# Optimization experiments

Hardware: AMD Instinct MI355X
Metric: run time of the kernel (lower is better)

Reference implementation:

```python
import jax, jax.numpy as jnp
import numpy as np

B, L, D, H, MAXREL = 8, 1024, 1024, 16, 32
DPH = D // H  # 64


def setup_inputs() -> dict:
    rng = jax.random.key(0)
    ks = jax.random.split(rng, 16)
    s = 0.02
    inp = {
        "key": jax.random.normal(ks[0], (B, L, D), jnp.float32),
        "value": jax.random.normal(ks[1], (B, L, D), jnp.float32),
        "query": jax.random.normal(ks[2], (B, L, D), jnp.float32),
        "mask": jax.random.bernoulli(ks[3], 0.1, (B, 1, L)),
        "Wq": jax.random.normal(ks[4], (D, D), jnp.float32) * s,
        "bq": jnp.zeros((D,), jnp.float32),
        "Wk": jax.random.normal(ks[5], (D, D), jnp.float32) * s,
        "bk": jnp.zeros((D,), jnp.float32),
        "Wv": jax.random.normal(ks[6], (D, D), jnp.float32) * s,
        "bv": jnp.zeros((D,), jnp.float32),
        "Wo": jax.random.normal(ks[7], (D, D), jnp.float32) * s,
        "bo": jnp.zeros((D,), jnp.float32),
        "rel_emb": jax.random.normal(ks[8], (2 * MAXREL + 1, DPH), jnp.float32) * s,
    }
    return inp


def reference(key, value, query, mask, Wq, bq, Wk, bk, Wv, bv, Wo, bo, rel_emb):
    b, l, d = query.shape
    def shape(x):  # (b, l, D) -> (b, H, l, dph)
        return x.reshape(b, -1, H, DPH).transpose(0, 2, 1, 3)

    q = shape(query @ Wq.T + bq) / jnp.sqrt(jnp.asarray(DPH, query.dtype))
    k = shape(key @ Wk.T + bk)
    v = shape(value @ Wv.T + bv)

    # Shaw-style relative position embeddings: rel[i, j] = clip(j - i, -M, M) + M
    idx = jnp.arange(l)
    rel = jnp.clip(idx[None, :] - idx[:, None], -MAXREL, MAXREL) + MAXREL  # (l, l)
    Er = rel_emb[rel]  # (l, l, dph) -- used for both keys and values (same table)

    scores = jnp.einsum('bhqd,bhkd->bhqk', q, k) + jnp.einsum('bhqd,qkd->bhqk', q, Er)
    scores = jnp.where(mask[:, None, :, :], jnp.asarray(-1e18, scores.dtype), scores)
    attn = jax.nn.softmax(scores, axis=-1)  # dropout = identity at eval

    ctx = jnp.einsum('bhqk,bhkd->bhqd', attn, v) + jnp.einsum('bhqk,qkd->bhqd', attn, Er)
    out = ctx.transpose(0, 2, 1, 3).reshape(b, l, H * DPH) @ Wo.T + bo
    top_attn = attn[:, 0]  # (b, q_len, k_len)
    return out, top_attn
```

## Files before the change

### kernel.cpp

```cpp
#include <hip/hip_runtime.h>
#include <hip/hip_bf16.h>

typedef __bf16 bf16x8 __attribute__((ext_vector_type(8)));
typedef __bf16 bf16x4 __attribute__((ext_vector_type(4)));
typedef float f32x4 __attribute__((ext_vector_type(4)));
typedef float f32x8 __attribute__((ext_vector_type(8)));

#define B_ 8
#define L_ 1024
#define D_ 1024
#define H_ 16
#define DPH_ 64
#define MAXREL_ 32
#define NREL_ 65

__device__ __forceinline__ f32x4 mfma16x16x32(bf16x8 a, bf16x8 b, f32x4 c) {
    return __builtin_amdgcn_mfma_f32_16x16x32_bf16(a, b, c, 0, 0, 0);
}

__device__ __forceinline__ bf16x8 ld_any(const float* p) {
    f32x8 v = *(const f32x8*)p;
    bf16x8 r;
    #pragma unroll
    for (int i = 0; i < 8; ++i) r[i] = (__bf16)v[i];
    return r;
}
__device__ __forceinline__ bf16x8 ld_any(const __bf16* p) { return *(const bf16x8*)p; }

template <int MODE, typename TA>
__global__ __launch_bounds__(512, 2) void gemm_v2(
    const TA* __restrict__ X, const float* __restrict__ Wt,
    const float* __restrict__ bias, void* __restrict__ outp,
    int M, int N, int K, float scale)
{
    __shared__ __bf16 sA[2][128 * 40];
    __shared__ __bf16 sB[2][256 * 40];

    const int tid = threadIdx.x;
    const int nbn = N >> 8;
    const int wg = (int)blockIdx.x;
    const int row0 = (wg / nbn) * 128, col0 = (wg % nbn) * 256;
    const int lane = tid & 63, w = tid >> 6, lr = lane & 15, lk = lane >> 4;
    const int wm = w >> 2, wn = w & 3;

    const int arow = tid >> 2, ak = (tid & 3) * 8;
    const int brow = tid >> 1, bk = (tid & 1) * 16;
    const TA*    agp = X  + (size_t)(row0 + arow) * K + ak;
    const float* bgp = Wt + (size_t)(col0 + brow) * K + bk;

    f32x4 acc[4][4];
    #pragma unroll
    for (int a = 0; a < 4; ++a)
        #pragma unroll
        for (int b = 0; b < 4; ++b) acc[a][b] = (f32x4){0.f, 0.f, 0.f, 0.f};

    f32x4 ra0, ra1;
    bf16x8 rab;
    f32x4 rb0, rb1, rb2, rb3;

    #define LOADG(t) do {                                                    \
        const int _k0 = (t) * 32;                                            \
        if (sizeof(TA) == 4) {                                               \
            ra0 = *(const f32x4*)((const float*)agp + _k0);                  \
            ra1 = *(const f32x4*)((const float*)agp + _k0 + 4);              \
        } else {                                                             \
            rab = *(const bf16x8*)((const __bf16*)agp + _k0);                \
        }                                                                    \
        rb0 = *(const f32x4*)(bgp + _k0);                                    \
        rb1 = *(const f32x4*)(bgp + _k0 + 4);                                \
        rb2 = *(const f32x4*)(bgp + _k0 + 8);                                \
        rb3 = *(const f32x4*)(bgp + _k0 + 12);                               \
    } while (0)

    #define WRITEL(buf) do {                                                 \
        bf16x8 _av;                                                          \
        if (sizeof(TA) == 4) {                                               \
            _Pragma("unroll")                                                \
            for (int i = 0; i < 4; ++i) {                                    \
                _av[i] = (__bf16)ra0[i]; _av[4 + i] = (__bf16)ra1[i];        \
            }                                                                \
        } else { _av = rab; }                                                \
        *(bf16x8*)&sA[buf][arow * 40 + ak] = _av;                            \
        bf16x8 _bv0, _bv1;                                                   \
        _Pragma("unroll")                                                    \
        for (int i = 0; i < 4; ++i) {                                        \
            _bv0[i] = (__bf16)rb0[i]; _bv0[4 + i] = (__bf16)rb1[i];          \
            _bv1[i] = (__bf16)rb2[i]; _bv1[4 + i] = (__bf16)rb3[i];          \
        }                                                                    \
        *(bf16x8*)&sB[buf][brow * 40 + bk]     = _bv0;                       \
        *(bf16x8*)&sB[buf][brow * 40 + bk + 8] = _bv1;                       \
    } while (0)

    LOADG(0);
    WRITEL(0);
    LOADG(1);
    __syncthreads();

    const int nkt = K >> 5;
    for (int t = 0; t < nkt; ++t) {
        const int cur = t & 1;
        bf16x8 af[4], bfr[4];
        #pragma unroll
        for (int m = 0; m < 4; ++m)
            af[m] = *(const bf16x8*)&sA[cur][(wm * 64 + m * 16 + lr) * 40 + 8 * lk];
        #pragma unroll
        for (int n = 0; n < 4; ++n)
            bfr[n] = *(const bf16x8*)&sB[cur][(wn * 64 + n * 16 + lr) * 40 + 8 * lk];
        __builtin_amdgcn_s_setprio(1);
        #pragma unroll
        for (int m = 0; m < 4; ++m)
            #pragma unroll
            for (int n = 0; n < 4; ++n)
                acc[m][n] = mfma16x16x32(af[m], bfr[n], acc[m][n]);
        __builtin_amdgcn_s_setprio(0);
        if (t < nkt - 1) {
            WRITEL(cur ^ 1);
            if (t < nkt - 2) LOADG(t + 2);
            __syncthreads();
        }
    }
    #undef LOADG
    #undef WRITEL

    #pragma unroll
    for (int ni = 0; ni < 4; ++ni) {
        const int n = col0 + wn * 64 + ni * 16 + lr;
        const float bv = bias[n];
        #pragma unroll
        for (int mi = 0; mi < 4; ++mi) {
            const int m0 = row0 + wm * 64 + mi * 16 + lk * 4;
            if (MODE == 0) {
                #pragma unroll
                for (int i = 0; i < 4; ++i)
                    ((__bf16*)outp)[(size_t)(m0 + i) * N + n] =
                        (__bf16)((acc[mi][ni][i] + bv) * scale);
            } else if (MODE == 1) {
                bf16x4 v4;
                #pragma unroll
                for (int i = 0; i < 4; ++i) v4[i] = (__bf16)(acc[mi][ni][i] + bv);
                *(bf16x4*)((__bf16*)outp + ((size_t)(m0 >> 10) << 20)
                           + (size_t)n * L_ + (m0 & 1023)) = v4;
            } else {
                #pragma unroll
                for (int i = 0; i < 4; ++i)
                    ((float*)outp)[(size_t)(m0 + i) * N + n] = acc[mi][ni][i] + bv;
            }
        }
    }
}

__global__ __launch_bounds__(256, 3) void attn_v5(
    const __bf16* __restrict__ Q, const __bf16* __restrict__ K,
    const __bf16* __restrict__ Vt, const int* __restrict__ mask,
    const float* __restrict__ relg, __bf16* __restrict__ ctx,
    float* __restrict__ attn0)
{
    __shared__ __bf16 sK[2][64 * 64];
    __shared__ __bf16 sV[2][64 * 64];
    __shared__ __bf16 s_rq[64 * 72];
    __shared__ __bf16 s_arel[64 * 72];
    __shared__ float s_sums[64];
    __shared__ unsigned s_mbits[32];

    const int tid = threadIdx.x;
    const int wg = ((int)blockIdx.x & 7) * 256 + ((int)blockIdx.x >> 3);
    const int qt = wg & 15, h = (wg >> 4) & 15, b = wg >> 8;
    const int q0 = qt * 64;
    const int lane = tid & 63, w = tid >> 6, lr = lane & 15, lk = lane >> 4;
    const size_t bh = (size_t)b * (L_ * D_) + (size_t)h * DPH_;
    const int qw = q0 + w * 16;
    const int ql = w * 16;

    const int strow = tid >> 3;
    const int scg   = (tid & 7) ^ (strow & 7);
    const __bf16* Kgp = K + bh + (size_t)strow * D_ + scg * 8;
    const __bf16* Vgp = Vt + ((size_t)b << 20)
                      + (size_t)(h * DPH_ + strow) * L_ + scg * 8;

    const __bf16* qp = Q + bh + (size_t)(qw + lr) * D_ + 8 * lk;
    const bf16x8 qf0 = *(const bf16x8*)qp;
    const bf16x8 qf1 = *(const bf16x8*)(qp + 32);

    #pragma unroll
    for (int rr = 0; rr < 4; ++rr) {
        const int k = rr * 256 + w * 64 + lane;
        const unsigned long long bal = __ballot(mask[b * L_ + k] != 0);
        if (lane == 0) {
            s_mbits[rr * 8 + w * 2]     = (unsigned)bal;
            s_mbits[rr * 8 + w * 2 + 1] = (unsigned)(bal >> 32);
        }
    }
    for (int i = tid; i < 64 * 72; i += 256) s_arel[i] = (__bf16)0.f;

    #pragma unroll
    for (int jt = 0; jt < 5; ++jt) {
        const int jr = jt * 16 + lr;
        const int jc = jr > 64 ? 64 : jr;
        const float* rp = relg + jc * 64 + 8 * lk;
        f32x4 rq = {0.f, 0.f, 0.f, 0.f};
        rq = mfma16x16x32(ld_any(rp), qf0, rq);
        rq = mfma16x16x32(ld_any(rp + 32), qf1, rq);
        #pragma unroll
        for (int i = 0; i < 4; ++i) {
            const int jj = jt * 16 + lk * 4 + i;
            if (jj <= 64) s_rq[(ql + lr) * 72 + jj] = (__bf16)rq[i];
        }
    }

    bf16x8 rk0 = *(const bf16x8*)(Kgp);
    bf16x8 rk1 = *(const bf16x8*)(Kgp + 32 * (size_t)D_);
    bf16x8 rv0 = *(const bf16x8*)(Vgp);
    bf16x8 rv1 = *(const bf16x8*)(Vgp + 32 * (size_t)L_);
    __syncthreads();

    const float rq0  = (float)s_rq[(ql + lr) * 72 + 0];
    const float rq64 = (float)s_rq[(ql + lr) * 72 + 64];

    float sum = 0.f, c0 = 0.f, c64 = 0.f;
    f32x4 pvacc[4];
    #pragma unroll
    for (int dt = 0; dt < 4; ++dt) pvacc[dt] = (f32x4){0.f, 0.f, 0.f, 0.f};
    float* a0p = attn0 + ((size_t)b * L_ + qw + lr) * L_;
    const int sw = lr & 7;
    const int s0l = lr + 32 * (lk & 1);
    const int s1l = s0l + 16;
    const bool hisel = (lk >> 1) != 0;

    for (int it = 0; it < 16; ++it) {
        const int cur = it & 1;
        const int k0 = it * 64;
        {
            __bf16* kd = &sK[cur][tid * 8];
            __bf16* vd = &sV[cur][tid * 8];
            *(bf16x8*)kd = rk0;  *(bf16x8*)(kd + 2048) = rk1;
            *(bf16x8*)vd = rv0;  *(bf16x8*)(vd + 2048) = rv1;
        }
        __syncthreads();
        if (it < 15) {
            const size_t ko = (size_t)(k0 + 64) * D_;
            rk0 = *(const bf16x8*)(Kgp + ko);
            rk1 = *(const bf16x8*)(Kgp + ko + 32 * (size_t)D_);
            rv0 = *(const bf16x8*)(Vgp + k0 + 64);
            rv1 = *(const bf16x8*)(Vgp + k0 + 64 + 32 * (size_t)L_);
        }

        const __bf16* kb = sK[cur];
        const __bf16* vb = sV[cur];

        float p[4][4];
        #pragma unroll
        for (int kt = 0; kt < 4; ++kt) {
            const int rb = (kt * 16 + lr) * 64;
            const bf16x8 a0 = *(const bf16x8*)&kb[rb + ((lk ^ sw) * 8)];
            const bf16x8 a1 = *(const bf16x8*)&kb[rb + (((lk + 4) ^ sw) * 8)];
            f32x4 acc = {0.f, 0.f, 0.f, 0.f};
            acc = mfma16x16x32(a0, qf0, acc);
            acc = mfma16x16x32(a1, qf1, acc);
            #pragma unroll
            for (int i = 0; i < 4; ++i) p[kt][i] = acc[i];
        }

        const unsigned mw0 = s_mbits[(k0 >> 5)];
        const unsigned mw1 = s_mbits[(k0 >> 5) + 1];
        const int side = (k0 <= qw - 95) ? -1 : ((k0 >= qw + 47) ? 1 : 0);
        if (side == 0) {
            #pragma unroll
            for (int kt = 0; kt < 4; ++kt) {
                const unsigned mword = kt < 2 ? mw0 : mw1;
                #pragma unroll
                for (int i = 0; i < 4; ++i) {
                    const int k = k0 + kt * 16 + lk * 4 + i;
                    const int dd = k - (qw + lr);
                    int j = dd + MAXREL_;
                    j = j < 0 ? 0 : (j > 64 ? 64 : j);
                    const float bias = (float)s_rq[(ql + lr) * 72 + j];
                    const float e = ((mword >> (k & 31)) & 1u)
                                  ? 0.f : __expf(p[kt][i] + bias);
                    p[kt][i] = e;
                    sum += e;
                    if (dd <= -MAXREL_)      c0  += e;
                    else if (dd >= MAXREL_)  c64 += e;
                    else s_arel[(ql + lr) * 72 + dd + MAXREL_] = (__bf16)e;
                }
            }
        } else {
            const float bias = side < 0 ? rq0 : rq64;
            float cacc = 0.f;
            #pragma unroll
            for (int kt = 0; kt < 4; ++kt) {
                const unsigned mword = kt < 2 ? mw0 : mw1;
                #pragma unroll
                for (int i = 0; i < 4; ++i) {
                    const int k = k0 + kt * 16 + lk * 4 + i;
                    const float e = ((mword >> (k & 31)) & 1u)
                                  ? 0.f : __expf(p[kt][i] + bias);
                    p[kt][i] = e;
                    cacc += e;
                }
            }
            sum += cacc;
            if (side < 0) c0 += cacc; else c64 += cacc;
        }

        if (h == 0) {
            #pragma unroll
            for (int kt = 0; kt < 4; ++kt) {
                f32x4 st;
                #pragma unroll
                for (int i = 0; i < 4; ++i) st[i] = p[kt][i];
                *(f32x4*)&a0p[k0 + kt * 16 + lk * 4] = st;
            }
        }

        unsigned pk[4][2];
        #pragma unroll
        for (int kt = 0; kt < 4; ++kt)
            #pragma unroll
            for (int hf = 0; hf < 2; ++hf) {
                union { unsigned u; __bf16 x[2]; } t;
                t.x[0] = (__bf16)p[kt][2 * hf];
                t.x[1] = (__bf16)p[kt][2 * hf + 1];
                pk[kt][hf] = t.u;
            }

        #pragma unroll
        for (int s = 0; s < 2; ++s) {
            union { unsigned u[4]; bf16x8 v; } ua;
            {
                const unsigned aE0 = __shfl((int)pk[2 * s][0],     s0l, 64);
                const unsigned aO0 = __shfl((int)pk[2 * s + 1][0], s0l, 64);
                const unsigned aE1 = __shfl((int)pk[2 * s][1],     s0l, 64);
                const unsigned aO1 = __shfl((int)pk[2 * s + 1][1], s0l, 64);
                const unsigned bE0 = __shfl((int)pk[2 * s][0],     s1l, 64);
                const unsigned bO0 = __shfl((int)pk[2 * s + 1][0], s1l, 64);
                const unsigned bE1 = __shfl((int)pk[2 * s][1],     s1l, 64);
                const unsigned bO1 = __shfl((int)pk[2 * s + 1][1], s1l, 64);
                ua.u[0] = hisel ? aO0 : aE0;
                ua.u[1] = hisel ? aO1 : aE1;
                ua.u[2] = hisel ? bO0 : bE0;
                ua.u[3] = hisel ? bO1 : bE1;
            }
            #pragma unroll
            for (int dt = 0; dt < 4; ++dt) {
                const bf16x8 bfv = *(const bf16x8*)
                    &vb[(dt * 16 + lr) * 64 + (((4 * s + lk) ^ sw) * 8)];
                pvacc[dt] = mfma16x16x32(ua.v, bfv, pvacc[dt]);
            }
        }
    }

    sum += __shfl_xor(sum, 16, 64); sum += __shfl_xor(sum, 32, 64);
    c0  += __shfl_xor(c0, 16, 64);  c0  += __shfl_xor(c0, 32, 64);
    c64 += __shfl_xor(c64, 16, 64); c64 += __shfl_xor(c64, 32, 64);
    if (lane < 16) {
        s_sums[ql + lr] = sum;
        s_arel[(ql + lr) * 72 + 0]  = (__bf16)c0;
        s_arel[(ql + lr) * 72 + 64] = (__bf16)c64;
    }
    __syncthreads();

    __bf16* rT = (__bf16*)sK;
    for (int i = tid; i < NREL_ * DPH_; i += 256)
        rT[(i & 63) * 72 + (i >> 6)] = (__bf16)relg[i];
    __syncthreads();

    const bf16x8 af1 = *(const bf16x8*)&s_arel[(ql + lr) * 72 + 8 * lk];
    const bf16x8 af2 = *(const bf16x8*)&s_arel[(ql + lr) * 72 + 32 + 8 * lk];
    float a64[4], inv[4];
    #pragma unroll
    for (int i = 0; i < 4; ++i) {
        a64[i] = (float)s_arel[(ql + lk * 4 + i) * 72 + 64];
        inv[i] = 1.f / s_sums[ql + lk * 4 + i];
    }
    #pragma unroll
    for (int dt = 0; dt < 4; ++dt) {
        const bf16x8 b1 = *(const bf16x8*)&rT[(dt * 16 + lr) * 72 + 8 * lk];
        const bf16x8 b2 = *(const bf16x8*)&rT[(dt * 16 + lr) * 72 + 32 + 8 * lk];
        pvacc[dt] = mfma16x16x32(af1, b1, pvacc[dt]);
        pvacc[dt] = mfma16x16x32(af2, b2, pvacc[dt]);
        const float r64 = (float)rT[(dt * 16 + lr) * 72 + 64];
        #pragma unroll
        for (int i = 0; i < 4; ++i) {
            const float outv = (pvacc[dt][i] + a64[i] * r64) * inv[i];
            ctx[((size_t)b * L_ + q0 + ql + lk * 4 + i) * D_
                + h * DPH_ + dt * 16 + lr] = (__bf16)outv;
        }
    }

    if (h == 0) {
        #pragma unroll 4
        for (int n = 0; n < 16; ++n) {
            const float invr = 1.f / s_sums[ql + n];
            float* ap = attn0 + ((size_t)b * L_ + q0 + ql + n) * L_ + lane * 16;
            #pragma unroll
            for (int c = 0; c < 4; ++c) {
                f32x4 v = *(f32x4*)&ap[c * 4];
                #pragma unroll
                for (int i = 0; i < 4; ++i) v[i] *= invr;
                *(f32x4*)&ap[c * 4] = v;
            }
        }
    }
}

extern "C" void kernel_launch(void* const* d_in, const int* in_sizes, int n_in,
                              void* d_out, int out_size, void* d_ws, size_t ws_size,
                              hipStream_t stream) {
    const float* key   = (const float*)d_in[0];
    const float* value = (const float*)d_in[1];
    const float* query = (const float*)d_in[2];
    const int*   mask  = (const int*)d_in[3];
    const float* Wq = (const float*)d_in[4];
    const float* bq = (const float*)d_in[5];
    const float* Wk = (const float*)d_in[6];
    const float* bk = (const float*)d_in[7];
    const float* Wv = (const float*)d_in[8];
    const float* bv = (const float*)d_in[9];
    const float* Wo = (const float*)d_in[10];
    const float* bo = (const float*)d_in[11];
    const float* relg = (const float*)d_in[12];

    float* out   = (float*)d_out;
    float* attn0 = out + (size_t)B_ * L_ * D_;

    char* ws = (char*)d_ws;
    __bf16* Qw   = (__bf16*)(ws);
    __bf16* Kw   = (__bf16*)(ws + ((size_t)16 << 20));
    __bf16* Vtw  = (__bf16*)(ws + ((size_t)32 << 20));
    __bf16* Ctxw = (__bf16*)(ws + ((size_t)48 << 20));

    const int M = B_ * L_;
    const int ngemm = (M / 128) * (D_ / 256);

    gemm_v2<0, float><<<ngemm, dim3(512), 0, stream>>>(query, Wq, bq, Qw, M, D_, D_, 0.125f);
    gemm_v2<0, float><<<ngemm, dim3(512), 0, stream>>>(key,   Wk, bk, Kw, M, D_, D_, 1.0f);
    gemm_v2<1, float><<<ngemm, dim3(512), 0, stream>>>(value, Wv, bv, Vtw, M, D_, D_, 1.0f);

    attn_v5<<<B_ * H_ * (L_ / 64), dim3(256), 0, stream>>>(
        Qw, Kw, Vtw, mask, relg, Ctxw, attn0);

    gemm_v2<2, __bf16><<<ngemm, dim3(512), 0, stream>>>(Ctxw, Wo, bo, out, M, D_, D_, 1.0f);
}
```

Baseline: 240.5 us.

## Process 128 query rows per attention block to reuse K/V tiles

The attention kernel now handles 128 queries per workgroup, each wave owning two 16-row query sub-tiles, so every K/V tile staged in shared memory feeds twice as many MFMAs. The grid halves to 1024 blocks and the launch bound drops to 2 waves per SIMD to fit the doubled accumulators and score registers. This cuts K/V global and LDS traffic per query but raises register and shared-memory pressure and lowers the number of resident blocks. The threshold for the far-right side test is also widened to cover the 32-row wave span.

```diff
diff --git a/kernel.cpp b/kernel.cpp
--- a/kernel.cpp
+++ b/kernel.cpp
@@ -149,7 +149,7 @@
     }
 }
 
-__global__ __launch_bounds__(256, 3) void attn_v5(
+__global__ __launch_bounds__(256, 2) void attn_v8(
     const __bf16* __restrict__ Q, const __bf16* __restrict__ K,
     const __bf16* __restrict__ Vt, const int* __restrict__ mask,
     const float* __restrict__ relg, __bf16* __restrict__ ctx,
@@ -157,19 +157,19 @@
 {
     __shared__ __bf16 sK[2][64 * 64];
     __shared__ __bf16 sV[2][64 * 64];
-    __shared__ __bf16 s_rq[64 * 72];
-    __shared__ __bf16 s_arel[64 * 72];
-    __shared__ float s_sums[64];
+    __shared__ __bf16 s_rq[128 * 72];
+    __shared__ __bf16 s_arel[128 * 72];
+    __shared__ float s_sums[128];
     __shared__ unsigned s_mbits[32];
 
     const int tid = threadIdx.x;
-    const int wg = ((int)blockIdx.x & 7) * 256 + ((int)blockIdx.x >> 3);
-    const int qt = wg & 15, h = (wg >> 4) & 15, b = wg >> 8;
-    const int q0 = qt * 64;
+    const int wg = ((int)blockIdx.x & 7) * 128 + ((int)blockIdx.x >> 3);
+    const int qt = wg & 7, h = (wg >> 3) & 15, b = wg >> 7;
+    const int q0 = qt * 128;
     const int lane = tid & 63, w = tid >> 6, lr = lane & 15, lk = lane >> 4;
     const size_t bh = (size_t)b * (L_ * D_) + (size_t)h * DPH_;
-    const int qw = q0 + w * 16;
-    const int ql = w * 16;
+    const int ql = w * 32;
+    const int qw = q0 + ql;
 
     const int strow = tid >> 3;
     const int scg   = (tid & 7) ^ (strow & 7);
@@ -177,9 +177,13 @@
     const __bf16* Vgp = Vt + ((size_t)b << 20)
                       + (size_t)(h * DPH_ + strow) * L_ + scg * 8;
 
-    const __bf16* qp = Q + bh + (size_t)(qw + lr) * D_ + 8 * lk;
-    const bf16x8 qf0 = *(const bf16x8*)qp;
-    const bf16x8 qf1 = *(const bf16x8*)(qp + 32);
+    bf16x8 qf[2][2];
+    #pragma unroll
+    for (int hf = 0; hf < 2; ++hf) {
+        const __bf16* qp = Q + bh + (size_t)(qw + hf * 16 + lr) * D_ + 8 * lk;
+        qf[hf][0] = *(const bf16x8*)qp;
+        qf[hf][1] = *(const bf16x8*)(qp + 32);
+    }
 
     #pragma unroll
     for (int rr = 0; rr < 4; ++rr) {
@@ -190,22 +194,24 @@
             s_mbits[rr * 8 + w * 2 + 1] = (unsigned)(bal >> 32);
         }
     }
-    for (int i = tid; i < 64 * 72; i += 256) s_arel[i] = (__bf16)0.f;
-
-    #pragma unroll
-    for (int jt = 0; jt < 5; ++jt) {
-        const int jr = jt * 16 + lr;
-        const int jc = jr > 64 ? 64 : jr;
-        const float* rp = relg + jc * 64 + 8 * lk;
-        f32x4 rq = {0.f, 0.f, 0.f, 0.f};
-        rq = mfma16x16x32(ld_any(rp), qf0, rq);
-        rq = mfma16x16x32(ld_any(rp + 32), qf1, rq);
-        #pragma unroll
-        for (int i = 0; i < 4; ++i) {
-            const int jj = jt * 16 + lk * 4 + i;
-            if (jj <= 64) s_rq[(ql + lr) * 72 + jj] = (__bf16)rq[i];
-        }
-    }
+    for (int i = tid; i < 128 * 72; i += 256) s_arel[i] = (__bf16)0.f;
+
+    #pragma unroll
+    for (int hf = 0; hf < 2; ++hf)
+        #pragma unroll
+        for (int jt = 0; jt < 5; ++jt) {
+            const int jr = jt * 16 + lr;
+            const int jc = jr > 64 ? 64 : jr;
+            const float* rp = relg + jc * 64 + 8 * lk;
+            f32x4 rq = {0.f, 0.f, 0.f, 0.f};
+            rq = mfma16x16x32(ld_any(rp), qf[hf][0], rq);
+            rq = mfma16x16x32(ld_any(rp + 32), qf[hf][1], rq);
+            #pragma unroll
+            for (int i = 0; i < 4; ++i) {
+                const int jj = jt * 16 + lk * 4 + i;
+                if (jj <= 64) s_rq[(ql + hf * 16 + lr) * 72 + jj] = (__bf16)rq[i];
+            }
+        }
 
     bf16x8 rk0 = *(const bf16x8*)(Kgp);
     bf16x8 rk1 = *(const bf16x8*)(Kgp + 32 * (size_t)D_);
@@ -213,14 +219,20 @@
     bf16x8 rv1 = *(const bf16x8*)(Vgp + 32 * (size_t)L_);
     __syncthreads();
 
-    const float rq0  = (float)s_rq[(ql + lr) * 72 + 0];
-    const float rq64 = (float)s_rq[(ql + lr) * 72 + 64];
-
-    float sum = 0.f, c0 = 0.f, c64 = 0.f;
-    f32x4 pvacc[4];
-    #pragma unroll
-    for (int dt = 0; dt < 4; ++dt) pvacc[dt] = (f32x4){0.f, 0.f, 0.f, 0.f};
-    float* a0p = attn0 + ((size_t)b * L_ + qw + lr) * L_;
+    float rq0[2], rq64[2];
+    #pragma unroll
+    for (int hf = 0; hf < 2; ++hf) {
+        rq0[hf]  = (float)s_rq[(ql + hf * 16 + lr) * 72 + 0];
+        rq64[hf] = (float)s_rq[(ql + hf * 16 + lr) * 72 + 64];
+    }
+
+    float sum0 = 0.f, sum1 = 0.f, c0a = 0.f, c0b = 0.f, c64a = 0.f, c64b = 0.f;
+    f32x4 pvA[4], pvB[4];
+    #pragma unroll
+    for (int dt = 0; dt < 4; ++dt) {
+        pvA[dt] = (f32x4){0.f, 0.f, 0.f, 0.f};
+        pvB[dt] = (f32x4){0.f, 0.f, 0.f, 0.f};
+    }
     const int sw = lr & 7;
     const int s0l = lr + 32 * (lk & 1);
     const int s1l = s0l + 16;
@@ -247,115 +259,147 @@
         const __bf16* kb = sK[cur];
         const __bf16* vb = sV[cur];
 
-        float p[4][4];
+        float p[2][4][4];
         #pragma unroll
         for (int kt = 0; kt < 4; ++kt) {
             const int rb = (kt * 16 + lr) * 64;
             const bf16x8 a0 = *(const bf16x8*)&kb[rb + ((lk ^ sw) * 8)];
             const bf16x8 a1 = *(const bf16x8*)&kb[rb + (((lk + 4) ^ sw) * 8)];
-            f32x4 acc = {0.f, 0.f, 0.f, 0.f};
-            acc = mfma16x16x32(a0, qf0, acc);
-            acc = mfma16x16x32(a1, qf1, acc);
-            #pragma unroll
-            for (int i = 0; i < 4; ++i) p[kt][i] = acc[i];
+            #pragma unroll
+            for (int hf = 0; hf < 2; ++hf) {
+                f32x4 acc = {0.f, 0.f, 0.f, 0.f};
+                acc = mfma16x16x32(a0, qf[hf][0], acc);
+                acc = mfma16x16x32(a1, qf[hf][1], acc);
+                #pragma unroll
+                for (int i = 0; i < 4; ++i) p[hf][kt][i] = acc[i];
+            }
         }
 
         const unsigned mw0 = s_mbits[(k0 >> 5)];
         const unsigned mw1 = s_mbits[(k0 >> 5) + 1];
-        const int side = (k0 <= qw - 95) ? -1 : ((k0 >= qw + 47) ? 1 : 0);
-        if (side == 0) {
-            #pragma unroll
-            for (int kt = 0; kt < 4; ++kt) {
-                const unsigned mword = kt < 2 ? mw0 : mw1;
-                #pragma unroll
-                for (int i = 0; i < 4; ++i) {
-                    const int k = k0 + kt * 16 + lk * 4 + i;
-                    const int dd = k - (qw + lr);
-                    int j = dd + MAXREL_;
-                    j = j < 0 ? 0 : (j > 64 ? 64 : j);
-                    const float bias = (float)s_rq[(ql + lr) * 72 + j];
-                    const float e = ((mword >> (k & 31)) & 1u)
-                                  ? 0.f : __expf(p[kt][i] + bias);
-                    p[kt][i] = e;
-                    sum += e;
-                    if (dd <= -MAXREL_)      c0  += e;
-                    else if (dd >= MAXREL_)  c64 += e;
-                    else s_arel[(ql + lr) * 72 + dd + MAXREL_] = (__bf16)e;
+        const int side = (k0 <= qw - 95) ? -1 : ((k0 >= qw + 63) ? 1 : 0);
+        #pragma unroll
+        for (int hf = 0; hf < 2; ++hf) {
+            const int qg = qw + hf * 16 + lr;
+            const int rqrow = (ql + hf * 16 + lr) * 72;
+            if (side == 0) {
+                float lsum = 0.f, lc0 = 0.f, lc64 = 0.f;
+                #pragma unroll
+                for (int kt = 0; kt < 4; ++kt) {
+                    const unsigned mword = kt < 2 ? mw0 : mw1;
+                    #pragma unroll
+                    for (int i = 0; i < 4; ++i) {
+                        const int k = k0 + kt * 16 + lk * 4 + i;
+                        const int dd = k - qg;
+                        int j = dd + MAXREL_;
+                        j = j < 0 ? 0 : (j > 64 ? 64 : j);
+                        const float bias = (float)s_rq[rqrow + j];
+                        const float e = ((mword >> (k & 31)) & 1u)
+                                      ? 0.f : __expf(p[hf][kt][i] + bias);
+                        p[hf][kt][i] = e;
+                        lsum += e;
+                        if (dd <= -MAXREL_)      lc0  += e;
+                        else if (dd >= MAXREL_)  lc64 += e;
+                        else s_arel[rqrow + dd + MAXREL_] = (__bf16)e;
+                    }
                 }
-            }
-        } else {
-            const float bias = side < 0 ? rq0 : rq64;
-            float cacc = 0.f;
-            #pragma unroll
-            for (int kt = 0; kt < 4; ++kt) {
-                const unsigned mword = kt < 2 ? mw0 : mw1;
-                #pragma unroll
-                for (int i = 0; i < 4; ++i) {
-                    const int k = k0 + kt * 16 + lk * 4 + i;
-                    const float e = ((mword >> (k & 31)) & 1u)
-                                  ? 0.f : __expf(p[kt][i] + bias);
-                    p[kt][i] = e;
-                    cacc += e;
+                if (hf == 0) { sum0 += lsum; c0a += lc0; c64a += lc64; }
+                else         { sum1 += lsum; c0b += lc0; c64b += lc64; }
+            } else {
+                const float bias = side < 0 ? rq0[hf] : rq64[hf];
+                float cacc = 0.f;
+                #pragma unroll
+                for (int kt = 0; kt < 4; ++kt) {
+                    const unsigned mword = kt < 2 ? mw0 : mw1;
+                    #pragma unroll
+                    for (int i = 0; i < 4; ++i) {
+                        const int k = k0 + kt * 16 + lk * 4 + i;
+                        const float e = ((mword >> (k & 31)) & 1u)
+                                      ? 0.f : __expf(p[hf][kt][i] + bias);
+                        p[hf][kt][i] = e;
+                        cacc += e;
+                    }
                 }
-            }
-            sum += cacc;
-            if (side < 0) c0 += cacc; else c64 += cacc;
+                if (hf == 0) {
+                    sum0 += cacc;
+                    if (side < 0) c0a += cacc; else c64a += cacc;
+                } else {
+                    sum1 += cacc;
+                    if (side < 0) c0b += cacc; else c64b += cacc;
+                }
+            }
         }
 
         if (h == 0) {
             #pragma unroll
-            for (int kt = 0; kt < 4; ++kt) {
-                f32x4 st;
-                #pragma unroll
-                for (int i = 0; i < 4; ++i) st[i] = p[kt][i];
-                *(f32x4*)&a0p[k0 + kt * 16 + lk * 4] = st;
-            }
-        }
-
-        unsigned pk[4][2];
-        #pragma unroll
-        for (int kt = 0; kt < 4; ++kt)
-            #pragma unroll
             for (int hf = 0; hf < 2; ++hf) {
-                union { unsigned u; __bf16 x[2]; } t;
-                t.x[0] = (__bf16)p[kt][2 * hf];
-                t.x[1] = (__bf16)p[kt][2 * hf + 1];
-                pk[kt][hf] = t.u;
-            }
+                float* a0p = attn0 + ((size_t)b * L_ + qw + hf * 16 + lr) * L_;
+                #pragma unroll
+                for (int kt = 0; kt < 4; ++kt) {
+                    f32x4 st;
+                    #pragma unroll
+                    for (int i = 0; i < 4; ++i) st[i] = p[hf][kt][i];
+                    *(f32x4*)&a0p[k0 + kt * 16 + lk * 4] = st;
+                }
+            }
+        }
+
+        unsigned pk[2][4][2];
+        #pragma unroll
+        for (int hf = 0; hf < 2; ++hf)
+            #pragma unroll
+            for (int kt = 0; kt < 4; ++kt)
+                #pragma unroll
+                for (int pf = 0; pf < 2; ++pf) {
+                    union { unsigned u; __bf16 x[2]; } t;
+                    t.x[0] = (__bf16)p[hf][kt][2 * pf];
+                    t.x[1] = (__bf16)p[hf][kt][2 * pf + 1];
+                    pk[hf][kt][pf] = t.u;
+                }
 
         #pragma unroll
         for (int s = 0; s < 2; ++s) {
-            union { unsigned u[4]; bf16x8 v; } ua;
-            {
-                const unsigned aE0 = __shfl((int)pk[2 * s][0],     s0l, 64);
-                const unsigned aO0 = __shfl((int)pk[2 * s + 1][0], s0l, 64);
-                const unsigned aE1 = __shfl((int)pk[2 * s][1],     s0l, 64);
-                const unsigned aO1 = __shfl((int)pk[2 * s + 1][1], s0l, 64);
-                const unsigned bE0 = __shfl((int)pk[2 * s][0],     s1l, 64);
-                const unsigned bO0 = __shfl((int)pk[2 * s + 1][0], s1l, 64);
-                const unsigned bE1 = __shfl((int)pk[2 * s][1],     s1l, 64);
-                const unsigned bO1 = __shfl((int)pk[2 * s + 1][1], s1l, 64);
-                ua.u[0] = hisel ? aO0 : aE0;
-                ua.u[1] = hisel ? aO1 : aE1;
-                ua.u[2] = hisel ? bO0 : bE0;
-                ua.u[3] = hisel ? bO1 : bE1;
+            union { unsigned u[4]; bf16x8 v; } uaA, uaB;
+            #pragma unroll
+            for (int hf = 0; hf < 2; ++hf) {
+                const unsigned aE0 = __shfl((int)pk[hf][2 * s][0],     s0l, 64);
+                const unsigned aO0 = __shfl((int)pk[hf][2 * s + 1][0], s0l, 64);
+                const unsigned aE1 = __shfl((int)pk[hf][2 * s][1],     s0l, 64);
+                const unsigned aO1 = __shfl((int)pk[hf][2 * s + 1][1], s0l, 64);
+                const unsigned bE0 = __shfl((int)pk[hf][2 * s][0],     s1l, 64);
+                const unsigned bO0 = __shfl((int)pk[hf][2 * s + 1][0], s1l, 64);
+                const unsigned bE1 = __shfl((int)pk[hf][2 * s][1],     s1l, 64);
+                const unsigned bO1 = __shfl((int)pk[hf][2 * s + 1][1], s1l, 64);
+                unsigned u0 = hisel ? aO0 : aE0;
+                unsigned u1 = hisel ? aO1 : aE1;
+                unsigned u2 = hisel ? bO0 : bE0;
+                unsigned u3 = hisel ? bO1 : bE1;
+                if (hf == 0) { uaA.u[0]=u0; uaA.u[1]=u1; uaA.u[2]=u2; uaA.u[3]=u3; }
+                else         { uaB.u[0]=u0; uaB.u[1]=u1; uaB.u[2]=u2; uaB.u[3]=u3; }
             }
             #pragma unroll
             for (int dt = 0; dt < 4; ++dt) {
                 const bf16x8 bfv = *(const bf16x8*)
                     &vb[(dt * 16 + lr) * 64 + (((4 * s + lk) ^ sw) * 8)];
-                pvacc[dt] = mfma16x16x32(ua.v, bfv, pvacc[dt]);
-            }
-        }
-    }
-
-    sum += __shfl_xor(sum, 16, 64); sum += __shfl_xor(sum, 32, 64);
-    c0  += __shfl_xor(c0, 16, 64);  c0  += __shfl_xor(c0, 32, 64);
-    c64 += __shfl_xor(c64, 16, 64); c64 += __shfl_xor(c64, 32, 64);
+                pvA[dt] = mfma16x16x32(uaA.v, bfv, pvA[dt]);
+                pvB[dt] = mfma16x16x32(uaB.v, bfv, pvB[dt]);
+            }
+        }
+    }
+
+    sum0 += __shfl_xor(sum0, 16, 64); sum0 += __shfl_xor(sum0, 32, 64);
+    sum1 += __shfl_xor(sum1, 16, 64); sum1 += __shfl_xor(sum1, 32, 64);
+    c0a  += __shfl_xor(c0a, 16, 64);  c0a  += __shfl_xor(c0a, 32, 64);
+    c0b  += __shfl_xor(c0b, 16, 64);  c0b  += __shfl_xor(c0b, 32, 64);
+    c64a += __shfl_xor(c64a, 16, 64); c64a += __shfl_xor(c64a, 32, 64);
+    c64b += __shfl_xor(c64b, 16, 64); c64b += __shfl_xor(c64b, 32, 64);
     if (lane < 16) {
-        s_sums[ql + lr] = sum;
-        s_arel[(ql + lr) * 72 + 0]  = (__bf16)c0;
-        s_arel[(ql + lr) * 72 + 64] = (__bf16)c64;
+        s_sums[ql + lr] = sum0;
+        s_sums[ql + 16 + lr] = sum1;
+        s_arel[(ql + lr) * 72 + 0]       = (__bf16)c0a;
+        s_arel[(ql + lr) * 72 + 64]      = (__bf16)c64a;
+        s_arel[(ql + 16 + lr) * 72 + 0]  = (__bf16)c0b;
+        s_arel[(ql + 16 + lr) * 72 + 64] = (__bf16)c64b;
     }
     __syncthreads();
 
@@ -364,32 +408,37 @@
         rT[(i & 63) * 72 + (i >> 6)] = (__bf16)relg[i];
     __syncthreads();
 
-    const bf16x8 af1 = *(const bf16x8*)&s_arel[(ql + lr) * 72 + 8 * lk];
-    const bf16x8 af2 = *(const bf16x8*)&s_arel[(ql + lr) * 72 + 32 + 8 * lk];
-    float a64[4], inv[4];
-    #pragma unroll
-    for (int i = 0; i < 4; ++i) {
-        a64[i] = (float)s_arel[(ql + lk * 4 + i) * 72 + 64];
-        inv[i] = 1.f / s_sums[ql + lk * 4 + i];
-    }
-    #pragma unroll
-    for (int dt = 0; dt < 4; ++dt) {
-        const bf16x8 b1 = *(const bf16x8*)&rT[(dt * 16 + lr) * 72 + 8 * lk];
-        const bf16x8 b2 = *(const bf16x8*)&rT[(dt * 16 + lr) * 72 + 32 + 8 * lk];
-        pvacc[dt] = mfma16x16x32(af1, b1, pvacc[dt]);
-        pvacc[dt] = mfma16x16x32(af2, b2, pvacc[dt]);
-        const float r64 = (float)rT[(dt * 16 + lr) * 72 + 64];
+    #pragma unroll
+    for (int hf = 0; hf < 2; ++hf) {
+        const int qrow = ql + hf * 16;
+        const bf16x8 af1 = *(const bf16x8*)&s_arel[(qrow + lr) * 72 + 8 * lk];
+        const bf16x8 af2 = *(const bf16x8*)&s_arel[(qrow + lr) * 72 + 32 + 8 * lk];
+        float a64[4], inv[4];
         #pragma unroll
         for (int i = 0; i < 4; ++i) {
-            const float outv = (pvacc[dt][i] + a64[i] * r64) * inv[i];
-            ctx[((size_t)b * L_ + q0 + ql + lk * 4 + i) * D_
-                + h * DPH_ + dt * 16 + lr] = (__bf16)outv;
+            a64[i] = (float)s_arel[(qrow + lk * 4 + i) * 72 + 64];
+            inv[i] = 1.f / s_sums[qrow + lk * 4 + i];
+        }
+        #pragma unroll
+        for (int dt = 0; dt < 4; ++dt) {
+            f32x4 pv = hf == 0 ? pvA[dt] : pvB[dt];
+            const bf16x8 b1 = *(const bf16x8*)&rT[(dt * 16 + lr) * 72 + 8 * lk];
+            const bf16x8 b2 = *(const bf16x8*)&rT[(dt * 16 + lr) * 72 + 32 + 8 * lk];
+            pv = mfma16x16x32(af1, b1, pv);
+            pv = mfma16x16x32(af2, b2, pv);
+            const float r64 = (float)rT[(dt * 16 + lr) * 72 + 64];
+            #pragma unroll
+            for (int i = 0; i < 4; ++i) {
+                const float outv = (pv[i] + a64[i] * r64) * inv[i];
+                ctx[((size_t)b * L_ + q0 + qrow + lk * 4 + i) * D_
+                    + h * DPH_ + dt * 16 + lr] = (__bf16)outv;
+            }
         }
     }
 
     if (h == 0) {
         #pragma unroll 4
-        for (int n = 0; n < 16; ++n) {
+        for (int n = 0; n < 32; ++n) {
             const float invr = 1.f / s_sums[ql + n];
             float* ap = attn0 + ((size_t)b * L_ + q0 + ql + n) * L_ + lane * 16;
             #pragma unroll
@@ -436,7 +485,7 @@
     gemm_v2<0, float><<<ngemm, dim3(512), 0, stream>>>(key,   Wk, bk, Kw, M, D_, D_, 1.0f);
     gemm_v2<1, float><<<ngemm, dim3(512), 0, stream>>>(value, Wv, bv, Vtw, M, D_, D_, 1.0f);
 
-    attn_v5<<<B_ * H_ * (L_ / 64), dim3(256), 0, stream>>>(
+    attn_v8<<<B_ * H_ * (L_ / 128), dim3(256), 0, stream>>>(
         Qw, Kw, Vtw, mask, relg, Ctxw, attn0);
 
     gemm_v2<2, __bf16><<<ngemm, dim3(512), 0, stream>>>(Ctxw, Wo, bo, out, M, D_, D_, 1.0f);
```

Measured after the change: 262.1 us. +9.0%, slower.

## Pre-convert weights to bf16 and fuse QKV projections into one XCD-aware launch

Applied to the files above, without the earlier changes.

Adds small kernels that convert Wq/Wk/Wv and Wo to bf16 into workspace each call. The three Q/K/V projection GEMMs are merged into one 768-block launch, with a block-to-tile mapping that groups tiles per XCD. The GEMM body is refactored into a device function that takes bf16 weights, which halves weight bytes loaded per tile and removes repeated fp32-to-bf16 conversion inside each GEMM block. The cost is extra conversion launches and workspace reuse: Wb aliases the Ctx buffer and Wob aliases the Q buffer, which relies on stream ordering to stay correct.

```diff
diff --git a/kernel.cpp b/kernel.cpp
--- a/kernel.cpp
+++ b/kernel.cpp
@@ -27,26 +27,47 @@
 }
 __device__ __forceinline__ bf16x8 ld_any(const __bf16* p) { return *(const bf16x8*)p; }
 
-template <int MODE, typename TA>
-__global__ __launch_bounds__(512, 2) void gemm_v2(
-    const TA* __restrict__ X, const float* __restrict__ Wt,
+__global__ __launch_bounds__(256) void cvt3(
+    const float* __restrict__ a, const float* __restrict__ b,
+    const float* __restrict__ c, __bf16* __restrict__ dst)
+{
+    const int gid = blockIdx.x * 256 + threadIdx.x;
+    const int arr = gid >> 17;
+    const int off = (gid & 131071) * 8;
+    const float* src = arr == 0 ? a : (arr == 1 ? b : c);
+    f32x8 v = *(const f32x8*)(src + off);
+    bf16x8 r;
+    #pragma unroll
+    for (int i = 0; i < 8; ++i) r[i] = (__bf16)v[i];
+    *(bf16x8*)(dst + ((size_t)arr << 20) + off) = r;
+}
+
+__global__ __launch_bounds__(256) void cvt1(
+    const float* __restrict__ a, __bf16* __restrict__ dst)
+{
+    const int off = (blockIdx.x * 256 + threadIdx.x) * 8;
+    f32x8 v = *(const f32x8*)(a + off);
+    bf16x8 r;
+    #pragma unroll
+    for (int i = 0; i < 8; ++i) r[i] = (__bf16)v[i];
+    *(bf16x8*)(dst + off) = r;
+}
+
+template <typename TA, typename TB>
+__device__ __forceinline__ void gemm_body(
+    const TA* __restrict__ X, const TB* __restrict__ Wt,
     const float* __restrict__ bias, void* __restrict__ outp,
-    int M, int N, int K, float scale)
+    const int row0, const int col0, const int mode, const float scale,
+    __bf16* sA, __bf16* sB)
 {
-    __shared__ __bf16 sA[2][128 * 40];
-    __shared__ __bf16 sB[2][256 * 40];
-
+    const int K = 1024, N = 1024;
     const int tid = threadIdx.x;
-    const int nbn = N >> 8;
-    const int wg = (int)blockIdx.x;
-    const int row0 = (wg / nbn) * 128, col0 = (wg % nbn) * 256;
     const int lane = tid & 63, w = tid >> 6, lr = lane & 15, lk = lane >> 4;
     const int wm = w >> 2, wn = w & 3;
-
     const int arow = tid >> 2, ak = (tid & 3) * 8;
     const int brow = tid >> 1, bk = (tid & 1) * 16;
-    const TA*    agp = X  + (size_t)(row0 + arow) * K + ak;
-    const float* bgp = Wt + (size_t)(col0 + brow) * K + bk;
+    const TA* agp = X  + (size_t)(row0 + arow) * K + ak;
+    const TB* bgp = Wt + (size_t)(col0 + brow) * K + bk;
 
     f32x4 acc[4][4];
     #pragma unroll
@@ -54,42 +75,47 @@
         #pragma unroll
         for (int b = 0; b < 4; ++b) acc[a][b] = (f32x4){0.f, 0.f, 0.f, 0.f};
 
-    f32x4 ra0, ra1;
-    bf16x8 rab;
-    f32x4 rb0, rb1, rb2, rb3;
-
-    #define LOADG(t) do {                                                    \
-        const int _k0 = (t) * 32;                                            \
-        if (sizeof(TA) == 4) {                                               \
-            ra0 = *(const f32x4*)((const float*)agp + _k0);                  \
-            ra1 = *(const f32x4*)((const float*)agp + _k0 + 4);              \
-        } else {                                                             \
-            rab = *(const bf16x8*)((const __bf16*)agp + _k0);                \
-        }                                                                    \
-        rb0 = *(const f32x4*)(bgp + _k0);                                    \
-        rb1 = *(const f32x4*)(bgp + _k0 + 4);                                \
-        rb2 = *(const f32x4*)(bgp + _k0 + 8);                                \
-        rb3 = *(const f32x4*)(bgp + _k0 + 12);                               \
-    } while (0)
-
-    #define WRITEL(buf) do {                                                 \
-        bf16x8 _av;                                                          \
-        if (sizeof(TA) == 4) {                                               \
-            _Pragma("unroll")                                                \
-            for (int i = 0; i < 4; ++i) {                                    \
-                _av[i] = (__bf16)ra0[i]; _av[4 + i] = (__bf16)ra1[i];        \
-            }                                                                \
-        } else { _av = rab; }                                                \
-        *(bf16x8*)&sA[buf][arow * 40 + ak] = _av;                            \
-        bf16x8 _bv0, _bv1;                                                   \
-        _Pragma("unroll")                                                    \
-        for (int i = 0; i < 4; ++i) {                                        \
-            _bv0[i] = (__bf16)rb0[i]; _bv0[4 + i] = (__bf16)rb1[i];          \
-            _bv1[i] = (__bf16)rb2[i]; _bv1[4 + i] = (__bf16)rb3[i];          \
-        }                                                                    \
-        *(bf16x8*)&sB[buf][brow * 40 + bk]     = _bv0;                       \
-        *(bf16x8*)&sB[buf][brow * 40 + bk + 8] = _bv1;                       \
-    } while (0)
+    f32x4 ra0, ra1; bf16x8 rab;
+    f32x4 rb0, rb1, rb2, rb3; bf16x8 rbb0, rbb1;
+
+    auto LOADG = [&](int t) {
+        const int k0 = t * 32;
+        if (sizeof(TA) == 4) {
+            ra0 = *(const f32x4*)((const float*)agp + k0);
+            ra1 = *(const f32x4*)((const float*)agp + k0 + 4);
+        } else {
+            rab = *(const bf16x8*)((const __bf16*)agp + k0);
+        }
+        if (sizeof(TB) == 4) {
+            rb0 = *(const f32x4*)((const float*)bgp + k0);
+            rb1 = *(const f32x4*)((const float*)bgp + k0 + 4);
+            rb2 = *(const f32x4*)((const float*)bgp + k0 + 8);
+            rb3 = *(const f32x4*)((const float*)bgp + k0 + 12);
+        } else {
+            rbb0 = *(const bf16x8*)((const __bf16*)bgp + k0);
+            rbb1 = *(const bf16x8*)((const __bf16*)bgp + k0 + 8);
+        }
+    };
+    auto WRITEL = [&](int buf) {
+        bf16x8 av;
+        if (sizeof(TA) == 4) {
+            #pragma unroll
+            for (int i = 0; i < 4; ++i) {
+                av[i] = (__bf16)ra0[i]; av[4 + i] = (__bf16)ra1[i];
+            }
+        } else av = rab;
+        *(bf16x8*)&sA[buf * (128 * 40) + arow * 40 + ak] = av;
+        bf16x8 bv0, bv1;
+        if (sizeof(TB) == 4) {
+            #pragma unroll
+            for (int i = 0; i < 4; ++i) {
+                bv0[i] = (__bf16)rb0[i]; bv0[4 + i] = (__bf16)rb1[i];
+                bv1[i] = (__bf16)rb2[i]; bv1[4 + i] = (__bf16)rb3[i];
+            }
+        } else { bv0 = rbb0; bv1 = rbb1; }
+        *(bf16x8*)&sB[buf * (256 * 40) + brow * 40 + bk]     = bv0;
+        *(bf16x8*)&sB[buf * (256 * 40) + brow * 40 + bk + 8] = bv1;
+    };
 
     LOADG(0);
     WRITEL(0);
@@ -102,10 +128,12 @@
         bf16x8 af[4], bfr[4];
         #pragma unroll
         for (int m = 0; m < 4; ++m)
-            af[m] = *(const bf16x8*)&sA[cur][(wm * 64 + m * 16 + lr) * 40 + 8 * lk];
+            af[m] = *(const bf16x8*)&sA[cur * (128 * 40)
+                     + (wm * 64 + m * 16 + lr) * 40 + 8 * lk];
         #pragma unroll
         for (int n = 0; n < 4; ++n)
-            bfr[n] = *(const bf16x8*)&sB[cur][(wn * 64 + n * 16 + lr) * 40 + 8 * lk];
+            bfr[n] = *(const bf16x8*)&sB[cur * (256 * 40)
+                     + (wn * 64 + n * 16 + lr) * 40 + 8 * lk];
         __builtin_amdgcn_s_setprio(1);
         #pragma unroll
         for (int m = 0; m < 4; ++m)
@@ -119,8 +147,6 @@
             __syncthreads();
         }
     }
-    #undef LOADG
-    #undef WRITEL
 
     #pragma unroll
     for (int ni = 0; ni < 4; ++ni) {
@@ -129,12 +155,12 @@
         #pragma unroll
         for (int mi = 0; mi < 4; ++mi) {
             const int m0 = row0 + wm * 64 + mi * 16 + lk * 4;
-            if (MODE == 0) {
+            if (mode == 0) {
                 #pragma unroll
                 for (int i = 0; i < 4; ++i)
                     ((__bf16*)outp)[(size_t)(m0 + i) * N + n] =
                         (__bf16)((acc[mi][ni][i] + bv) * scale);
-            } else if (MODE == 1) {
+            } else if (mode == 1) {
                 bf16x4 v4;
                 #pragma unroll
                 for (int i = 0; i < 4; ++i) v4[i] = (__bf16)(acc[mi][ni][i] + bv);
@@ -147,6 +173,39 @@
             }
         }
     }
+}
+
+__global__ __launch_bounds__(512, 2) void gemm_qkv_fused(
+    const float* __restrict__ Xq, const float* __restrict__ Xk,
+    const float* __restrict__ Xv, const __bf16* __restrict__ Wb,
+    const float* __restrict__ bq, const float* __restrict__ bk,
+    const float* __restrict__ bv,
+    __bf16* __restrict__ Qw, __bf16* __restrict__ Kw, __bf16* __restrict__ Vtw)
+{
+    __shared__ __bf16 sA[2 * 128 * 40];
+    __shared__ __bf16 sB[2 * 256 * 40];
+    const int bid = (int)blockIdx.x;
+    const int xcd = bid & 7, idx = bid >> 3;
+    const int z = idx >> 5, t = idx & 31;
+    const int tile = xcd * 32 + t;
+    const int row0 = (tile >> 2) * 128, col0 = (tile & 3) * 256;
+    const float* X = z == 0 ? Xq : (z == 1 ? Xk : Xv);
+    const __bf16* Wt = Wb + ((size_t)z << 20);
+    const float* bias = z == 0 ? bq : (z == 1 ? bk : bv);
+    void* outp = z == 0 ? (void*)Qw : (z == 1 ? (void*)Kw : (void*)Vtw);
+    gemm_body<float, __bf16>(X, Wt, bias, outp, row0, col0,
+                             z == 2 ? 1 : 0, z == 0 ? 0.125f : 1.0f, sA, sB);
+}
+
+__global__ __launch_bounds__(512, 2) void gemm_out_k(
+    const __bf16* __restrict__ X, const __bf16* __restrict__ Wt,
+    const float* __restrict__ bias, float* __restrict__ outp)
+{
+    __shared__ __bf16 sA[2 * 128 * 40];
+    __shared__ __bf16 sB[2 * 256 * 40];
+    const int wg = (int)blockIdx.x;
+    const int row0 = (wg >> 2) * 128, col0 = (wg & 3) * 256;
+    gemm_body<__bf16, __bf16>(X, Wt, bias, outp, row0, col0, 2, 1.0f, sA, sB);
 }
 
 __global__ __launch_bounds__(256, 3) void attn_v5(
@@ -428,16 +487,17 @@
     __bf16* Kw   = (__bf16*)(ws + ((size_t)16 << 20));
     __bf16* Vtw  = (__bf16*)(ws + ((size_t)32 << 20));
     __bf16* Ctxw = (__bf16*)(ws + ((size_t)48 << 20));
-
-    const int M = B_ * L_;
-    const int ngemm = (M / 128) * (D_ / 256);
-
-    gemm_v2<0, float><<<ngemm, dim3(512), 0, stream>>>(query, Wq, bq, Qw, M, D_, D_, 0.125f);
-    gemm_v2<0, float><<<ngemm, dim3(512), 0, stream>>>(key,   Wk, bk, Kw, M, D_, D_, 1.0f);
-    gemm_v2<1, float><<<ngemm, dim3(512), 0, stream>>>(value, Wv, bv, Vtw, M, D_, D_, 1.0f);
+    __bf16* Wb   = (__bf16*)(ws + ((size_t)48 << 20));
+    __bf16* Wob  = (__bf16*)(ws);
+
+    cvt3<<<1536, 256, 0, stream>>>(Wq, Wk, Wv, Wb);
+
+    gemm_qkv_fused<<<768, dim3(512), 0, stream>>>(
+        query, key, value, Wb, bq, bk, bv, Qw, Kw, Vtw);
 
     attn_v5<<<B_ * H_ * (L_ / 64), dim3(256), 0, stream>>>(
         Qw, Kw, Vtw, mask, relg, Ctxw, attn0);
 
-    gemm_v2<2, __bf16><<<ngemm, dim3(512), 0, stream>>>(Ctxw, Wo, bo, out, M, D_, D_, 1.0f);
-}
+    cvt1<<<512, 256, 0, stream>>>(Wo, Wob);
+    gemm_out_k<<<256, dim3(512), 0, stream>>>(Ctxw, Wob, bo, out);
+}
```

New measurement: 230.4 us. -4.2%, faster.
